# Optimization experiments

Measured on AMD Instinct MI355X. Metric: run time of the kernel, lower is better.

The kernel has to match this reference:

```python
import jax, jax.numpy as jnp
import numpy as np
from jax import lax

NUM_GROUPS = 16
GN_EPS = 1e-5
POOL = 4
CLAMP_MIN, CLAMP_MAX = 0.0, 1.0


def setup_inputs() -> dict:
    key = jax.random.key(0)
    ks = jax.random.split(key, 4)
    x = jax.random.normal(ks[0], (128, 8, 128, 128), dtype=jnp.float32)
    conv_weight = jax.random.normal(ks[1], (64, 8, 3, 3), dtype=jnp.float32) * 0.1
    conv_bias = jax.random.normal(ks[2], (64,), dtype=jnp.float32) * 0.1
    gn_weight = jnp.ones((64,), dtype=jnp.float32)
    gn_bias = jnp.zeros((64,), dtype=jnp.float32)
    scale = jax.random.normal(ks[3], (64, 1, 1), dtype=jnp.float32)
    return {"x": x, "conv_weight": conv_weight, "conv_bias": conv_bias,
            "gn_weight": gn_weight, "gn_bias": gn_bias, "scale": scale}


def reference(x, conv_weight, conv_bias, gn_weight, gn_bias, scale):
    # Conv2d (stride=1, padding=0)
    y = lax.conv_general_dilated(
        x, conv_weight, window_strides=(1, 1), padding='VALID',
        dimension_numbers=('NCHW', 'OIHW', 'NCHW'))
    y = y + conv_bias[None, :, None, None]  # [B, C, H, W] = [128, 64, 126, 126]

    # GroupNorm over (channels-in-group, H, W) per sample
    B, C, H, W = y.shape
    yg = y.reshape(B, NUM_GROUPS, C // NUM_GROUPS, H, W)
    mean = jnp.mean(yg, axis=(2, 3, 4), keepdims=True)
    var = jnp.var(yg, axis=(2, 3, 4), keepdims=True)
    yn = ((yg - mean) * lax.rsqrt(var + GN_EPS)).reshape(B, C, H, W)
    yn = yn * gn_weight[None, :, None, None] + gn_bias[None, :, None, None]

    # scale (broadcast [C,1,1])
    yn = yn * scale[None]

    # MaxPool2d(kernel=4, stride=4)
    p = lax.reduce_window(yn, -jnp.inf, lax.max,
                          window_dimensions=(1, 1, POOL, POOL),
                          window_strides=(1, 1, POOL, POOL),
                          padding='VALID')  # [128, 64, 31, 31]

    # clamp
    return jnp.clip(p, CLAMP_MIN, CLAMP_MAX)
```

## Files before the change

kernel.cpp:

```cpp
#include <hip/hip_runtime.h>
#include <math.h>

typedef _Float16 f16x8 __attribute__((ext_vector_type(8)));
typedef float f32x4 __attribute__((ext_vector_type(4)));

#define CIN 8
#define HIN 128
#define WIN 128
#define OH 126
#define OW 126
#define COUT 64
#define NB 128
#define NGROUPS 16
#define CPG 4
#define PWN 31
#define XROWS 34
#define XH_DIM 130
#define TPIX (34*34)

#define XH_BYTES   ((size_t)NB*XH_DIM*XH_DIM*CIN*2)
#define WEXT_BYTES ((size_t)NB*PWN*PWN*COUT*2)
#define PART_BYTES ((size_t)NB*NGROUPS*4*2*4)
#define WS_NEEDED  (XH_BYTES + WEXT_BYTES + PART_BYTES)

#define NPOOL (NB*PWN*PWN*COUT)
#define OFF_PART_OLD (NPOOL/2)

__global__ __launch_bounds__(192)
void xpack_kernel(const float* __restrict__ x, _Float16* __restrict__ xh)
{
  const int iy = blockIdx.x;
  const int b  = blockIdx.y;
  const int ix = threadIdx.x;
  if (ix >= XH_DIM) return;
  f16x8 pk = {0,0,0,0,0,0,0,0};
  if (iy < HIN && ix < WIN) {
    const float* xb = x + (size_t)b*CIN*HIN*WIN + iy*WIN + ix;
    #pragma unroll
    for (int ci = 0; ci < 8; ++ci)
      pk[ci] = (_Float16)xb[ci*HIN*WIN];
  }
  *(f16x8*)&xh[(((size_t)b*XH_DIM + iy)*XH_DIM + ix)*CIN] = pk;
}

__global__ __launch_bounds__(512)
void conv_dma_kernel(const _Float16* __restrict__ xh,
                     const float* __restrict__ w,
                     const float* __restrict__ bias,
                     const float* __restrict__ gnw,
                     const float* __restrict__ scale,
                     _Float16* __restrict__ wext,
                     float* __restrict__ parts)
{
  __shared__ __align__(16) _Float16 xs[2][TPIX*8];
  __shared__ __align__(16) _Float16 wls[9*64*8];
  __shared__ float red[8][16][2];

  const int tid  = threadIdx.x;
  const int lane = tid & 63, wave = tid >> 6;
  const int tx = blockIdx.x;
  const int b  = blockIdx.y;
  const int ox0 = tx*32;

  for (int idx = tid; idx < 9*64*8; idx += 512) {
    const int ci = idx & 7, n = (idx >> 3) & 63, khw = idx >> 9;
    wls[idx] = (_Float16)w[(n*CIN + ci)*9 + khw];
  }

  const int q = lane >> 4, ln = lane & 15;

  auto stage = [&](int buf, int ty) {
    const int oy0 = ty*32;
    #pragma unroll
    for (int k = 0; k < 3; ++k) {
      const int p = k*512 + tid;
      if (p < TPIX) {
        const int r = p / 34, c = p - r*34;
        const size_t gb = (((size_t)b*XH_DIM + (oy0 + r))*XH_DIM + (ox0 + c))*CIN;
        __builtin_amdgcn_global_load_lds(
            (const __attribute__((address_space(1))) void*)(xh + gb),
            (__attribute__((address_space(3))) void*)&xs[buf][p*8],
            16, 0, 0);
      }
    }
  };

  stage(0, 0);

  asm volatile("s_waitcnt vmcnt(0)" ::: "memory");
  __syncthreads();

  f16x8 bf[4][3];
  #pragma unroll
  for (int nt = 0; nt < 4; ++nt) {
    #pragma unroll
    for (int c = 0; c < 2; ++c)
      bf[nt][c] = *(const f16x8*)&wls[((c*4 + q)*64 + nt*16 + ln)*8];
    if (q == 0)
      bf[nt][2] = *(const f16x8*)&wls[((8)*64 + nt*16 + ln)*8];
    else
      bf[nt][2] = (f16x8){0,0,0,0,0,0,0,0};
  }

  const int dy = ln >> 2, dx = ln & 3;
  int aoff[3];
  #pragma unroll
  for (int c = 0; c < 3; ++c) {
    const int khw = c*4 + q;
    const int ky = khw / 3, kx = khw - 3*(khw/3);
    aoff[c] = (khw < 9) ? ((dy + ky)*34 + (dx + kx))*8 : 0;
  }

  float bias_r[4], sgn[4];
  #pragma unroll
  for (int nt = 0; nt < 4; ++nt) {
    const int c = nt*16 + ln;
    bias_r[nt] = bias[c];
    sgn[nt] = (gnw[c]*scale[c] >= 0.f) ? 1.f : -1.f;
  }

  float s[4]  = {0.f,0.f,0.f,0.f};
  float sq[4] = {0.f,0.f,0.f,0.f};

  for (int ty = 0; ty < 4; ++ty) {
    const int cur = ty & 1;
    if (ty < 3) stage(cur ^ 1, ty + 1);

    #pragma unroll 2
    for (int i = 0; i < 8; ++i) {
      const int wxl = i;
      const int base = (wave*4*34 + wxl*4)*8;

      f32x4 acc[4];
      #pragma unroll
      for (int nt = 0; nt < 4; ++nt) {
        const float bv = bias_r[nt];
        acc[nt] = (f32x4){bv, bv, bv, bv};
      }
      #pragma unroll
      for (int c = 0; c < 3; ++c) {
        const f16x8 a = *(const f16x8*)&xs[cur][base + aoff[c]];
        #pragma unroll
        for (int nt = 0; nt < 4; ++nt)
          acc[nt] = __builtin_amdgcn_mfma_f32_16x16x32_f16(a, bf[nt][c], acc[nt], 0, 0, 0);
      }

      const int wyg = ty*8 + wave, wxg = tx*8 + wxl;
      if ((wyg < PWN) && (wxg < PWN)) {
        const size_t rowbase = ((size_t)(b*PWN + wyg)*PWN + wxg)*COUT;
        float m4[4];
        #pragma unroll
        for (int nt = 0; nt < 4; ++nt) {
          const float v0 = acc[nt][0], v1 = acc[nt][1];
          const float v2 = acc[nt][2], v3 = acc[nt][3];
          s[nt]  += (v0+v1) + (v2+v3);
          sq[nt] += v0*v0 + v1*v1 + v2*v2 + v3*v3;
          const float sg = sgn[nt];
          float m = fmaxf(fmaxf(sg*v0, sg*v1), fmaxf(sg*v2, sg*v3));
          m = fmaxf(m, __shfl_xor(m, 16, 64));
          m = fmaxf(m, __shfl_xor(m, 32, 64));
          m4[nt] = sg*m;
        }
        float mv = m4[0];
        mv = (q == 1) ? m4[1] : mv;
        mv = (q == 2) ? m4[2] : mv;
        mv = (q == 3) ? m4[3] : mv;
        wext[rowbase + lane] = (_Float16)mv;
      } else {
        const bool yv = (wyg*4 + q) < OH;
        #pragma unroll
        for (int nt = 0; nt < 4; ++nt) {
          #pragma unroll
          for (int r = 0; r < 4; ++r) {
            const bool okp = yv && (wxg*4 + r < OW);
            const float v = okp ? acc[nt][r] : 0.f;
            s[nt] += v; sq[nt] += v*v;
          }
        }
      }
    }

    if (ty < 3) {
      asm volatile("s_waitcnt vmcnt(0)" ::: "memory");
      __syncthreads();
    }
  }

  #pragma unroll
  for (int nt = 0; nt < 4; ++nt) {
    float a = s[nt], c2 = sq[nt];
    a  += __shfl_xor(a, 16, 64);  a  += __shfl_xor(a, 32, 64);
    a  += __shfl_xor(a, 1, 64);   a  += __shfl_xor(a, 2, 64);
    c2 += __shfl_xor(c2, 16, 64); c2 += __shfl_xor(c2, 32, 64);
    c2 += __shfl_xor(c2, 1, 64);  c2 += __shfl_xor(c2, 2, 64);
    if (lane < 16 && (lane & 3) == 0) {
      red[wave][nt*4 + (ln >> 2)][0] = a;
      red[wave][nt*4 + (ln >> 2)][1] = c2;
    }
  }
  __syncthreads();
  if (tid < 32) {
    const int g = tid >> 1, k = tid & 1;
    float t = 0.f;
    #pragma unroll
    for (int wv = 0; wv < 8; ++wv) t += red[wv][g][k];
    parts[(((size_t)b*NGROUPS + g)*4 + tx)*2 + k] = t;
  }
}

__global__ __launch_bounds__(256)
void conv_mfma_kernel(const float* __restrict__ x,
                      const float* __restrict__ w,
                      const float* __restrict__ bias,
                      const float* __restrict__ gnw,
                      const float* __restrict__ scale,
                      float* __restrict__ ws)
{
  __shared__ __align__(16) _Float16 xs[XROWS*34*8];
  __shared__ __align__(16) _Float16 wls[9*64*8];
  __shared__ float red[4][16][2];

  const int tid  = threadIdx.x;
  const int lane = tid & 63, wave = tid >> 6;
  const int tileIdx = blockIdx.x;
  const int tx = tileIdx & 3, ty = tileIdx >> 2;
  const int b  = blockIdx.y;
  const int ox0 = tx*32, oy0 = ty*32;

  for (int idx = tid; idx < 9*64*8; idx += 256) {
    const int ci = idx & 7, n = (idx >> 3) & 63, khw = idx >> 9;
    wls[idx] = (_Float16)w[(n*CIN + ci)*9 + khw];
  }
  const float* xb = x + (size_t)b * CIN*HIN*WIN;
  for (int p = tid; p < XROWS*34; p += 256) {
    const int r = p / 34, c = p - r*34;
    const int iy = oy0 + r, ix = ox0 + c;
    const bool ok = (iy < HIN) && (ix < WIN);
    const int gbase = iy*WIN + ix;
    f16x8 pk;
    #pragma unroll
    for (int ci = 0; ci < 8; ++ci) {
      const float v = ok ? xb[ci*HIN*WIN + gbase] : 0.f;
      pk[ci] = (_Float16)v;
    }
    *(f16x8*)&xs[p*8] = pk;
  }
  __syncthreads();

  const int q = lane >> 4, ln = lane & 15;
  f16x8 bf[4][3];
  #pragma unroll
  for (int nt = 0; nt < 4; ++nt) {
    #pragma unroll
    for (int c = 0; c < 2; ++c)
      bf[nt][c] = *(const f16x8*)&wls[((c*4 + q)*64 + nt*16 + ln)*8];
    if (q == 0) bf[nt][2] = *(const f16x8*)&wls[((8)*64 + nt*16 + ln)*8];
    else        bf[nt][2] = (f16x8){0,0,0,0,0,0,0,0};
  }
  const int dy = ln >> 2, dx = ln & 3;
  int aoff[3];
  #pragma unroll
  for (int c = 0; c < 3; ++c) {
    const int khw = c*4 + q;
    const int ky = khw / 3, kx = khw - 3*(khw/3);
    aoff[c] = (khw < 9) ? ((dy + ky)*34 + (dx + kx))*8 : 0;
  }
  float bias_r[4], sgn[4];
  #pragma unroll
  for (int nt = 0; nt < 4; ++nt) {
    const int c = nt*16 + ln;
    bias_r[nt] = bias[c];
    sgn[nt] = (gnw[c]*scale[c] >= 0.f) ? 1.f : -1.f;
  }
  float s[4]  = {0.f,0.f,0.f,0.f};
  float sq[4] = {0.f,0.f,0.f,0.f};
  _Float16* wext = (_Float16*)ws;

  #pragma unroll 2
  for (int i = 0; i < 16; ++i) {
    const int wyl = wave*2 + (i >> 3), wxl = i & 7;
    const int base = (wyl*4*34 + wxl*4)*8;
    f32x4 acc[4];
    #pragma unroll
    for (int nt = 0; nt < 4; ++nt) {
      const float bv = bias_r[nt];
      acc[nt] = (f32x4){bv, bv, bv, bv};
    }
    #pragma unroll
    for (int c = 0; c < 3; ++c) {
      const f16x8 a = *(const f16x8*)&xs[base + aoff[c]];
      #pragma unroll
      for (int nt = 0; nt < 4; ++nt)
        acc[nt] = __builtin_amdgcn_mfma_f32_16x16x32_f16(a, bf[nt][c], acc[nt], 0, 0, 0);
    }
    const int wyg = ty*8 + wyl, wxg = tx*8 + wxl;
    if ((wyg < PWN) && (wxg < PWN)) {
      const size_t rowbase = ((size_t)(b*PWN + wyg)*PWN + wxg)*COUT;
      float m4[4];
      #pragma unroll
      for (int nt = 0; nt < 4; ++nt) {
        const float v0 = acc[nt][0], v1 = acc[nt][1];
        const float v2 = acc[nt][2], v3 = acc[nt][3];
        s[nt]  += (v0+v1) + (v2+v3);
        sq[nt] += v0*v0 + v1*v1 + v2*v2 + v3*v3;
        const float sg = sgn[nt];
        float m = fmaxf(fmaxf(sg*v0, sg*v1), fmaxf(sg*v2, sg*v3));
        m = fmaxf(m, __shfl_xor(m, 16, 64));
        m = fmaxf(m, __shfl_xor(m, 32, 64));
        m4[nt] = sg*m;
      }
      float mv = m4[0];
      mv = (q == 1) ? m4[1] : mv;
      mv = (q == 2) ? m4[2] : mv;
      mv = (q == 3) ? m4[3] : mv;
      wext[rowbase + lane] = (_Float16)mv;
    } else {
      const bool yv = (wyg*4 + q) < OH;
      #pragma unroll
      for (int nt = 0; nt < 4; ++nt) {
        #pragma unroll
        for (int r = 0; r < 4; ++r) {
          const bool okp = yv && (wxg*4 + r < OW);
          const float v = okp ? acc[nt][r] : 0.f;
          s[nt] += v; sq[nt] += v*v;
        }
      }
    }
  }
  #pragma unroll
  for (int nt = 0; nt < 4; ++nt) {
    float a = s[nt], c2 = sq[nt];
    a  += __shfl_xor(a, 16, 64);  a  += __shfl_xor(a, 32, 64);
    a  += __shfl_xor(a, 1, 64);   a  += __shfl_xor(a, 2, 64);
    c2 += __shfl_xor(c2, 16, 64); c2 += __shfl_xor(c2, 32, 64);
    c2 += __shfl_xor(c2, 1, 64);  c2 += __shfl_xor(c2, 2, 64);
    if (lane < 16 && (lane & 3) == 0) {
      red[wave][nt*4 + (ln >> 2)][0] = a;
      red[wave][nt*4 + (ln >> 2)][1] = c2;
    }
  }
  __syncthreads();
  if (tid < 32) {
    const int g = tid >> 1, k = tid & 1;
    const float t = red[0][g][k] + red[1][g][k] + red[2][g][k] + red[3][g][k];
    ws[OFF_PART_OLD + (((size_t)b*NGROUPS + g)*16 + tileIdx)*2 + k] = t;
  }
}

__global__ __launch_bounds__(256)
void tail_kernel(const float* __restrict__ gnw,
                 const float* __restrict__ gnb,
                 const float* __restrict__ scale,
                 const _Float16* __restrict__ wext,
                 const float* __restrict__ parts,
                 const int nparts,
                 float* __restrict__ out)
{
  __shared__ float stat[NGROUPS*2];
  __shared__ float AB[128];
  __shared__ float vout[COUT*PWN];

  const int tid = threadIdx.x;
  const int xb  = blockIdx.x;
  const int b   = blockIdx.y;

  if (tid < 32) {
    const int g = tid >> 1, k = tid & 1;
    const float* p = parts + ((size_t)(b*NGROUPS + g)*nparts)*2 + k;
    float a = 0.f;
    for (int t = 0; t < nparts; ++t) a += p[t*2];
    stat[g*2 + k] = a;
  }
  __syncthreads();
  if (tid < COUT) {
    const int c = tid, g = c >> 2;
    const float N = (float)(CPG * OH * OW);
    const float mean = stat[g*2] / N;
    const float var  = stat[g*2 + 1] / N - mean*mean;
    const float inv  = rsqrtf(var + 1e-5f);
    const float ag   = inv * gnw[c];
    AB[c]      = ag * scale[c];
    AB[64 + c] = (gnb[c] - mean * ag) * scale[c];
  }
  __syncthreads();

  #pragma unroll
  for (int r = 0; r < 2; ++r) {
    const int wy = xb*2 + r;
    if (wy >= PWN) break;
    const size_t rb = (size_t)(b*PWN + wy)*PWN*COUT;

    if (tid < 248) {
      const f16x8 e = *(const f16x8*)&wext[rb + tid*8];
      const int wx = tid >> 3, c0 = (tid & 7)*8;
      #pragma unroll
      for (int j = 0; j < 8; ++j) {
        const int c = c0 + j;
        float v = fmaf(AB[c], (float)e[j], AB[64 + c]);
        v = fminf(fmaxf(v, 0.f), 1.f);
        vout[c*PWN + wx] = v;
      }
    }
    __syncthreads();
    for (int e = tid; e < COUT*PWN; e += 256) {
      const int c = e / PWN, wx = e - c*PWN;
      out[(((size_t)b*COUT + c)*PWN + wy)*PWN + wx] = vout[e];
    }
    __syncthreads();
  }
}

extern "C" void kernel_launch(void* const* d_in, const int* in_sizes, int n_in,
                              void* d_out, int out_size, void* d_ws, size_t ws_size,
                              hipStream_t stream)
{
  const float* x     = (const float*)d_in[0];
  const float* cw    = (const float*)d_in[1];
  const float* cb    = (const float*)d_in[2];
  const float* gnw   = (const float*)d_in[3];
  const float* gnb   = (const float*)d_in[4];
  const float* scale = (const float*)d_in[5];
  float* out = (float*)d_out;
  float* ws  = (float*)d_ws;

  if (ws_size >= WS_NEEDED) {
    _Float16* xh   = (_Float16*)ws;
    _Float16* wext = (_Float16*)((char*)ws + XH_BYTES);
    float*    prt  = (float*)((char*)ws + XH_BYTES + WEXT_BYTES);

    xpack_kernel<<<dim3(XH_DIM, NB), 192, 0, stream>>>(x, xh);
    conv_dma_kernel<<<dim3(4, NB), 512, 0, stream>>>(xh, cw, cb, gnw, scale, wext, prt);
    tail_kernel<<<dim3(16, NB), 256, 0, stream>>>(gnw, gnb, scale, wext, prt, 4, out);
  } else {
    conv_mfma_kernel<<<dim3(16, NB), 256, 0, stream>>>(x, cw, cb, gnw, scale, ws);
    tail_kernel<<<dim3(16, NB), 256, 0, stream>>>(gnw, gnb, scale,
                                                  (const _Float16*)ws,
                                                  ws + OFF_PART_OLD, 16, out);
  }
}
```

Baseline: 177.0 us.

## Remap conv MFMA tiles to row-strips and pre-pack fp16 weights globally

The conv kernel now maps each MFMA's 16 M-rows to 16 consecutive pixels along a row instead of a 4x4 pool window. Each wave loops over 4 rows and accumulates the pooled max in registers, which removes the per-tile cross-lane shuffles and the branchy edge handling. Pooled results go through a small LDS buffer so they can be written as vectorized 8-byte stores. Weight conversion to fp16 moves into an extra block of the pack kernel, so each conv block loads B fragments straight from global memory instead of rebuilding the weight LDS table. In exchange, the x tile in LDS is padded by 3072 halfs per buffer, the masking logic becomes more involved, and an early break skips rows past the output edge.

```diff
diff --git a/kernel.cpp b/kernel.cpp
--- a/kernel.cpp
+++ b/kernel.cpp
@@ -17,20 +17,31 @@
 #define XROWS 34
 #define XH_DIM 130
 #define TPIX (34*34)
+#define XSPAD 3072
 
 #define XH_BYTES   ((size_t)NB*XH_DIM*XH_DIM*CIN*2)
 #define WEXT_BYTES ((size_t)NB*PWN*PWN*COUT*2)
 #define PART_BYTES ((size_t)NB*NGROUPS*4*2*4)
-#define WS_NEEDED  (XH_BYTES + WEXT_BYTES + PART_BYTES)
+#define WH_BYTES   ((size_t)9*64*8*2)
+#define WS_NEEDED  (XH_BYTES + WEXT_BYTES + PART_BYTES + WH_BYTES)
 
 #define NPOOL (NB*PWN*PWN*COUT)
 #define OFF_PART_OLD (NPOOL/2)
 
 __global__ __launch_bounds__(192)
-void xpack_kernel(const float* __restrict__ x, _Float16* __restrict__ xh)
+void xpack_kernel(const float* __restrict__ x, const float* __restrict__ w,
+                  _Float16* __restrict__ xh, _Float16* __restrict__ wh)
 {
   const int iy = blockIdx.x;
   const int b  = blockIdx.y;
+  if (iy == XH_DIM) {
+    if (b != 0) return;
+    for (int i = threadIdx.x; i < 9*64*8; i += 192) {
+      const int khw = i >> 9, rem = i & 511;
+      wh[i] = (_Float16)w[rem*9 + khw];
+    }
+    return;
+  }
   const int ix = threadIdx.x;
   if (ix >= XH_DIM) return;
   f16x8 pk = {0,0,0,0,0,0,0,0};
@@ -45,27 +56,22 @@
 
 __global__ __launch_bounds__(512)
 void conv_dma_kernel(const _Float16* __restrict__ xh,
-                     const float* __restrict__ w,
+                     const _Float16* __restrict__ wh,
                      const float* __restrict__ bias,
                      const float* __restrict__ gnw,
                      const float* __restrict__ scale,
                      _Float16* __restrict__ wext,
                      float* __restrict__ parts)
 {
-  __shared__ __align__(16) _Float16 xs[2][TPIX*8];
-  __shared__ __align__(16) _Float16 wls[9*64*8];
+  __shared__ __align__(16) _Float16 xs[2][TPIX*8 + XSPAD];
+  __shared__ __align__(8)  _Float16 sbuf[8][256];
   __shared__ float red[8][16][2];
 
   const int tid  = threadIdx.x;
-  const int lane = tid & 63, wave = tid >> 6;
+  const int lane = tid & 63, wv = tid >> 6;
   const int tx = blockIdx.x;
   const int b  = blockIdx.y;
   const int ox0 = tx*32;
-
-  for (int idx = tid; idx < 9*64*8; idx += 512) {
-    const int ci = idx & 7, n = (idx >> 3) & 63, khw = idx >> 9;
-    wls[idx] = (_Float16)w[(n*CIN + ci)*9 + khw];
-  }
 
   const int q = lane >> 4, ln = lane & 15;
 
@@ -87,28 +93,24 @@
 
   stage(0, 0);
 
-  asm volatile("s_waitcnt vmcnt(0)" ::: "memory");
-  __syncthreads();
-
   f16x8 bf[4][3];
   #pragma unroll
   for (int nt = 0; nt < 4; ++nt) {
     #pragma unroll
     for (int c = 0; c < 2; ++c)
-      bf[nt][c] = *(const f16x8*)&wls[((c*4 + q)*64 + nt*16 + ln)*8];
+      bf[nt][c] = *(const f16x8*)&wh[((c*4 + q)*64 + nt*16 + ln)*8];
     if (q == 0)
-      bf[nt][2] = *(const f16x8*)&wls[((8)*64 + nt*16 + ln)*8];
+      bf[nt][2] = *(const f16x8*)&wh[((8)*64 + nt*16 + ln)*8];
     else
       bf[nt][2] = (f16x8){0,0,0,0,0,0,0,0};
   }
 
-  const int dy = ln >> 2, dx = ln & 3;
   int aoff[3];
   #pragma unroll
   for (int c = 0; c < 3; ++c) {
     const int khw = c*4 + q;
     const int ky = khw / 3, kx = khw - 3*(khw/3);
-    aoff[c] = (khw < 9) ? ((dy + ky)*34 + (dx + kx))*8 : 0;
+    aoff[c] = (khw < 9) ? (ky*34 + kx + ln)*8 : ln*8;
   }
 
   float bias_r[4], sgn[4];
@@ -122,60 +124,67 @@
   float s[4]  = {0.f,0.f,0.f,0.f};
   float sq[4] = {0.f,0.f,0.f,0.f};
 
+  const float xm_hi = (q < 3) ? 1.f : 0.f;
+
+  asm volatile("s_waitcnt vmcnt(0)" ::: "memory");
+  __syncthreads();
+
   for (int ty = 0; ty < 4; ++ty) {
     const int cur = ty & 1;
     if (ty < 3) stage(cur ^ 1, ty + 1);
 
-    #pragma unroll 2
-    for (int i = 0; i < 8; ++i) {
-      const int wxl = i;
-      const int base = (wave*4*34 + wxl*4)*8;
-
-      f32x4 acc[4];
+    const int wy_g = ty*8 + wv;
+    const int oy0  = ty*32;
+
+    #pragma unroll
+    for (int bd = 0; bd < 2; ++bd) {
+      const int x0 = bd << 4;
+      const bool xedge = (tx == 3) && (bd == 1);
+
+      float mx[4] = {-1e30f, -1e30f, -1e30f, -1e30f};
+
       #pragma unroll
-      for (int nt = 0; nt < 4; ++nt) {
-        const float bv = bias_r[nt];
-        acc[nt] = (f32x4){bv, bv, bv, bv};
-      }
-      #pragma unroll
-      for (int c = 0; c < 3; ++c) {
-        const f16x8 a = *(const f16x8*)&xs[cur][base + aoff[c]];
-        #pragma unroll
-        for (int nt = 0; nt < 4; ++nt)
-          acc[nt] = __builtin_amdgcn_mfma_f32_16x16x32_f16(a, bf[nt][c], acc[nt], 0, 0, 0);
-      }
-
-      const int wyg = ty*8 + wave, wxg = tx*8 + wxl;
-      if ((wyg < PWN) && (wxg < PWN)) {
-        const size_t rowbase = ((size_t)(b*PWN + wyg)*PWN + wxg)*COUT;
-        float m4[4];
+      for (int sy = 0; sy < 4; ++sy) {
+        const int y_l = wv*4 + sy;
+        if (oy0 + y_l >= OH) break;
+        const int base = (y_l*34 + x0)*8;
+
+        f32x4 acc[4];
         #pragma unroll
         for (int nt = 0; nt < 4; ++nt) {
-          const float v0 = acc[nt][0], v1 = acc[nt][1];
-          const float v2 = acc[nt][2], v3 = acc[nt][3];
+          const float bv = bias_r[nt];
+          acc[nt] = (f32x4){bv, bv, bv, bv};
+        }
+        #pragma unroll
+        for (int c = 0; c < 3; ++c) {
+          const f16x8 a = *(const f16x8*)&xs[cur][base + aoff[c]];
+          #pragma unroll
+          for (int nt = 0; nt < 4; ++nt)
+            acc[nt] = __builtin_amdgcn_mfma_f32_16x16x32_f16(a, bf[nt][c], acc[nt], 0, 0, 0);
+        }
+
+        #pragma unroll
+        for (int nt = 0; nt < 4; ++nt) {
+          float v0 = acc[nt][0], v1 = acc[nt][1];
+          float v2 = acc[nt][2], v3 = acc[nt][3];
+          if (xedge) { v2 *= xm_hi; v3 *= xm_hi; }
           s[nt]  += (v0+v1) + (v2+v3);
           sq[nt] += v0*v0 + v1*v1 + v2*v2 + v3*v3;
           const float sg = sgn[nt];
-          float m = fmaxf(fmaxf(sg*v0, sg*v1), fmaxf(sg*v2, sg*v3));
-          m = fmaxf(m, __shfl_xor(m, 16, 64));
-          m = fmaxf(m, __shfl_xor(m, 32, 64));
-          m4[nt] = sg*m;
+          const float m = fmaxf(fmaxf(sg*v0, sg*v1), fmaxf(sg*v2, sg*v3));
+          mx[nt] = fmaxf(mx[nt], m);
         }
-        float mv = m4[0];
-        mv = (q == 1) ? m4[1] : mv;
-        mv = (q == 2) ? m4[2] : mv;
-        mv = (q == 3) ? m4[3] : mv;
-        wext[rowbase + lane] = (_Float16)mv;
-      } else {
-        const bool yv = (wyg*4 + q) < OH;
+      }
+
+      if (wy_g < PWN) {
         #pragma unroll
-        for (int nt = 0; nt < 4; ++nt) {
-          #pragma unroll
-          for (int r = 0; r < 4; ++r) {
-            const bool okp = yv && (wxg*4 + r < OW);
-            const float v = okp ? acc[nt][r] : 0.f;
-            s[nt] += v; sq[nt] += v*v;
-          }
+        for (int nt = 0; nt < 4; ++nt)
+          sbuf[wv][q*64 + nt*16 + ln] = (_Float16)(sgn[nt]*mx[nt]);
+        const int nw = xedge ? 3 : 4;
+        if (lane < nw*16) {
+          const int wx0_g = tx*8 + (x0 >> 2);
+          const uint2 v = *(const uint2*)&sbuf[wv][lane*4];
+          *(uint2*)&wext[(((size_t)b*PWN + wy_g)*PWN + wx0_g)*COUT + lane*4] = v;
         }
       }
     }
@@ -194,8 +203,8 @@
     c2 += __shfl_xor(c2, 16, 64); c2 += __shfl_xor(c2, 32, 64);
     c2 += __shfl_xor(c2, 1, 64);  c2 += __shfl_xor(c2, 2, 64);
     if (lane < 16 && (lane & 3) == 0) {
-      red[wave][nt*4 + (ln >> 2)][0] = a;
-      red[wave][nt*4 + (ln >> 2)][1] = c2;
+      red[wv][nt*4 + (ln >> 2)][0] = a;
+      red[wv][nt*4 + (ln >> 2)][1] = c2;
     }
   }
   __syncthreads();
@@ -203,7 +212,7 @@
     const int g = tid >> 1, k = tid & 1;
     float t = 0.f;
     #pragma unroll
-    for (int wv = 0; wv < 8; ++wv) t += red[wv][g][k];
+    for (int w8 = 0; w8 < 8; ++w8) t += red[w8][g][k];
     parts[(((size_t)b*NGROUPS + g)*4 + tx)*2 + k] = t;
   }
 }
@@ -427,9 +436,10 @@
     _Float16* xh   = (_Float16*)ws;
     _Float16* wext = (_Float16*)((char*)ws + XH_BYTES);
     float*    prt  = (float*)((char*)ws + XH_BYTES + WEXT_BYTES);
-
-    xpack_kernel<<<dim3(XH_DIM, NB), 192, 0, stream>>>(x, xh);
-    conv_dma_kernel<<<dim3(4, NB), 512, 0, stream>>>(xh, cw, cb, gnw, scale, wext, prt);
+    _Float16* wh   = (_Float16*)((char*)ws + XH_BYTES + WEXT_BYTES + PART_BYTES);
+
+    xpack_kernel<<<dim3(XH_DIM + 1, NB), 192, 0, stream>>>(x, cw, xh, wh);
+    conv_dma_kernel<<<dim3(4, NB), 512, 0, stream>>>(xh, wh, cb, gnw, scale, wext, prt);
     tail_kernel<<<dim3(16, NB), 256, 0, stream>>>(gnw, gnb, scale, wext, prt, 4, out);
   } else {
     conv_mfma_kernel<<<dim3(16, NB), 256, 0, stream>>>(x, cw, cb, gnw, scale, ws);
```

Measured after the change: 167.2 us. 5.5% less time.
